# Kernel tuning notes

Measured on AMD Instinct MI355X. Metric: run time of the kernel, lower is better.

The kernel has to match this reference:

```python
import jax, jax.numpy as jnp
import numpy as np


def _dwconv(x, w, pad):
    # x: [B,C,H,W], w: [C,1,kh,kw] depthwise conv (groups=C), no bias
    return jax.lax.conv_general_dilated(
        x, w, window_strides=(1, 1), padding=[(pad, pad), (pad, pad)],
        dimension_numbers=('NCHW', 'OIHW', 'NCHW'),
        feature_group_count=x.shape[1])


def _omni_shift(x, alpha, cw1, cw3, cw5):
    # OmniShift training branch: alpha-weighted identity + 1x1 + 3x3 + 5x5 depthwise convs
    return (alpha[0] * x + alpha[1] * _dwconv(x, cw1, 0)
            + alpha[2] * _dwconv(x, cw3, 1) + alpha[3] * _dwconv(x, cw5, 2))


def _wkv(w_dec, u, k, v):
    # Numerically-stable RWKV-v4 WKV recurrence. w_dec,u: [D]; k,v: [B,T,D]
    kT = jnp.swapaxes(k, 0, 1)  # [T,B,D]
    vT = jnp.swapaxes(v, 0, 1)
    z = jnp.zeros_like(k[:, 0])
    init = (z, z, jnp.full_like(z, -1e38))  # (a, b, running max exponent)

    def step(carry, kv):
        a, b, pp = carry
        kt, vt = kv
        ww = u + kt
        p = jnp.maximum(pp, ww)
        e1 = jnp.exp(pp - p)
        e2 = jnp.exp(ww - p)
        out = (e1 * a + e2 * vt) / (e1 * b + e2)
        ww2 = pp + w_dec
        p2 = jnp.maximum(ww2, kt)
        f1 = jnp.exp(ww2 - p2)
        f2 = jnp.exp(kt - p2)
        return (f1 * a + f2 * vt, f1 * b + f2, p2), out

    _, out = jax.lax.scan(step, init, (kT, vT))
    return jnp.swapaxes(out, 0, 1)


def _forward(x, alpha, cw1, cw3, cw5, Wk, Wv, Wr, Wo, spatial_decay, spatial_first, h, w):
    B, T, C = x.shape
    xi = x.reshape(B, h, w, C).transpose(0, 3, 1, 2)  # b (h w) c -> b c h w
    xi = _omni_shift(xi, alpha, cw1, cw3, cw5)
    xf = xi.transpose(0, 2, 3, 1).reshape(B, T, C)    # b c h w -> b (h w) c
    k = jnp.einsum('btc,oc->bto', xf, Wk)
    v = jnp.einsum('btc,oc->bto', xf, Wv)
    r = jnp.einsum('btc,oc->bto', xf, Wr)
    sr = jax.nn.sigmoid(r)
    # 'b (h w) c -> b (w h) c' : W-major reordering for the second scan direction
    k1 = k.reshape(B, h, w, C).transpose(0, 2, 1, 3).reshape(B, T, C)
    v1 = v.reshape(B, h, w, C).transpose(0, 2, 1, 3).reshape(B, T, C)
    ks = jnp.concatenate([k, k1], axis=2)   # [B,T,2C]
    vs = jnp.concatenate([v, v1], axis=2)
    srs = jnp.concatenate([sr, sr], axis=2)
    w_dec = -jnp.exp(spatial_decay / T)  # WKV kernel applies w = -exp(w)
    u = spatial_first / T
    xs = _wkv(w_dec, u, ks, vs)
    xs = xs * srs
    return jnp.einsum('btd,cd->btc', xs, Wo)  # output Linear(2C -> C), no bias


def setup_inputs() -> dict:
    key = jax.random.key(0)
    ks = jax.random.split(key, 11)
    B, h, w, C = 8, 64, 64, 256
    T = h * w
    s = 0.02
    return {
        'x': jax.random.normal(ks[0], (B, T, C), jnp.float32),
        'alpha': jax.random.normal(ks[1], (4,), jnp.float32),
        'cw1': jax.random.normal(ks[2], (C, 1, 1, 1), jnp.float32) * s,
        'cw3': jax.random.normal(ks[3], (C, 1, 3, 3), jnp.float32) * s,
        'cw5': jax.random.normal(ks[4], (C, 1, 5, 5), jnp.float32) * s,
        'Wk': jax.random.normal(ks[5], (C, C), jnp.float32) * s,
        'Wv': jax.random.normal(ks[6], (C, C), jnp.float32) * s,
        'Wr': jax.random.normal(ks[7], (C, C), jnp.float32) * s,
        'Wo': jax.random.normal(ks[8], (C, 2 * C), jnp.float32) * s,
        'spatial_decay': jax.random.normal(ks[9], (2 * C,), jnp.float32),
        'spatial_first': jax.random.normal(ks[10], (2 * C,), jnp.float32),
        'h': h,
        'w': w,
    }


def reference(x, alpha, cw1, cw3, cw5, Wk, Wv, Wr, Wo, spatial_decay, spatial_first, h, w):
    return _forward(x, alpha, cw1, cw3, cw5, Wk, Wv, Wr, Wo, spatial_decay, spatial_first, h, w)
```

## Files before the change

### kernel.cpp

```cpp
#include <hip/hip_runtime.h>
#include <math.h>
#include <stdint.h>

#define TT 4096
#define HH 64
#define WW 64
#define CC 256
#define NCH 64
#define LCH 64

typedef __bf16 bf16x8 __attribute__((ext_vector_type(8)));
typedef float  f32x4  __attribute__((ext_vector_type(4)));

__device__ __forceinline__ unsigned short f2bf(float x) {
    uint32_t u = __float_as_uint(x);
    u = (u + 0x7fffu + ((u >> 16) & 1u)) >> 16;
    return (unsigned short)u;
}
__device__ __forceinline__ float bf2f(unsigned short h) {
    return __uint_as_float(((uint32_t)h) << 16);
}

__global__ __launch_bounds__(256)
void prep_all(const float* __restrict__ alpha,
              const float* __restrict__ cw1,
              const float* __restrict__ cw3,
              const float* __restrict__ cw5,
              const float* __restrict__ Wk, const float* __restrict__ Wv,
              const float* __restrict__ Wr, const float* __restrict__ Wo,
              float* __restrict__ weff,
              unsigned short* __restrict__ W2k, unsigned short* __restrict__ W2v,
              unsigned short* __restrict__ W2r, unsigned short* __restrict__ Wo2,
              int do_wo) {
    int bid = blockIdx.x, c = threadIdx.x;
    if (bid < 25) {
        int k = bid;
        float a0 = alpha[0], a1 = alpha[1], a2 = alpha[2], a3 = alpha[3];
        float v = a3 * cw5[c * 25 + k];
        int ky = k / 5, kx = k % 5;
        if (ky >= 1 && ky <= 3 && kx >= 1 && kx <= 3)
            v += a2 * cw3[c * 9 + (ky - 1) * 3 + (kx - 1)];
        if (k == 12) v += a1 * cw1[c] + a0;
        weff[k * CC + c] = v;
    } else if (bid < 281) {
        int n = bid - 25;
        float a;
        unsigned short h;
        a = Wk[n * 256 + c]; h = f2bf(a); W2k[n * 512 + c] = h; W2k[n * 512 + 256 + c] = f2bf(a - bf2f(h));
        a = Wv[n * 256 + c]; h = f2bf(a); W2v[n * 512 + c] = h; W2v[n * 512 + 256 + c] = f2bf(a - bf2f(h));
        a = Wr[n * 256 + c]; h = f2bf(a); W2r[n * 512 + c] = h; W2r[n * 512 + 256 + c] = f2bf(a - bf2f(h));
    } else if (do_wo) {
        int n = bid - 281;
        float a = Wo[n * 512 + c];
        unsigned short h = f2bf(a);
        Wo2[n * 1024 + c] = h; Wo2[n * 1024 + 256 + c] = f2bf(a - bf2f(h));
        float b = Wo[n * 512 + 256 + c];
        unsigned short h2 = f2bf(b);
        Wo2[n * 1024 + 512 + c] = h2; Wo2[n * 1024 + 768 + c] = f2bf(b - bf2f(h2));
    }
}

__global__ __launch_bounds__(256)
void prep_wo(const float* __restrict__ Wo, unsigned short* __restrict__ Wo2) {
    int n = blockIdx.x, c = threadIdx.x;
    float a = Wo[n * 512 + c];
    unsigned short h = f2bf(a);
    Wo2[n * 1024 + c] = h; Wo2[n * 1024 + 256 + c] = f2bf(a - bf2f(h));
    float b = Wo[n * 512 + 256 + c];
    unsigned short h2 = f2bf(b);
    Wo2[n * 1024 + 512 + c] = h2; Wo2[n * 1024 + 768 + c] = f2bf(b - bf2f(h2));
}

__global__ __launch_bounds__(256)
void omni_conv(const float* __restrict__ x,
               const float* __restrict__ weff,
               unsigned short* __restrict__ A2) {
    int xx = blockIdx.x;
    int y0 = blockIdx.y * 32;
    int b  = blockIdx.z;
    int c  = threadIdx.x;
    const float* xb = x + (size_t)b * TT * CC + c;
    unsigned short* Ab = A2 + (size_t)b * TT * 512 + c;

    float wk[25];
    #pragma unroll
    for (int k = 0; k < 25; ++k) wk[k] = weff[k * CC + c];

    float win[5][5];
    #pragma unroll
    for (int i = 0; i < 4; ++i) {
        int yy = y0 - 2 + i;
        #pragma unroll
        for (int dx = 0; dx < 5; ++dx) {
            int xc = xx + dx - 2;
            win[i][dx] = (yy >= 0 && xc >= 0 && xc < WW)
                         ? xb[(size_t)(yy * WW + xc) * CC] : 0.f;
        }
    }
    #pragma unroll
    for (int i = 0; i < 32; ++i) {
        int y = y0 + i;
        int yy = y + 2;
        #pragma unroll
        for (int dx = 0; dx < 5; ++dx) {
            int xc = xx + dx - 2;
            win[4][dx] = (yy < HH && xc >= 0 && xc < WW)
                         ? xb[(size_t)(yy * WW + xc) * CC] : 0.f;
        }
        float acc = 0.f;
        #pragma unroll
        for (int r = 0; r < 5; ++r)
            #pragma unroll
            for (int dx = 0; dx < 5; ++dx)
                acc = fmaf(wk[r * 5 + dx], win[r][dx], acc);
        unsigned short h = f2bf(acc);
        size_t o = (size_t)(y * WW + xx) * 512;
        Ab[o] = h;
        Ab[o + 256] = f2bf(acc - bf2f(h));
        #pragma unroll
        for (int r = 0; r < 4; ++r)
            #pragma unroll
            for (int dx = 0; dx < 5; ++dx)
                win[r][dx] = win[r + 1][dx];
    }
}

template<int KIND>
__device__ __forceinline__ void mfma_core(const unsigned short* __restrict__ A0,
                                          const unsigned short* __restrict__ A1,
                                          const unsigned short* __restrict__ W2,
                                          float* __restrict__ C,
                                          int m_blk, int n_blk, bool act) {
    __shared__ __align__(16) unsigned short L[2][4][128 * 32];
    int tid = threadIdx.x;
    int w = tid >> 6, l = tid & 63;
    int q = l >> 4, rr = l & 15;
    int wm = (w & 1) * 64, wn = (w >> 1) * 64;
    int srw = w * 16 + (l >> 2);
    int ss  = l & 3;

    const int NCHK = (KIND == 0) ? 8 : 16;
    const int LDW  = (KIND == 0) ? 512 : 1024;

    f32x4 acc[4][4];
    #pragma unroll
    for (int i = 0; i < 4; ++i)
        #pragma unroll
        for (int j = 0; j < 4; ++j)
            acc[i][j] = (f32x4){0.f, 0.f, 0.f, 0.f};

    auto stage = [&](int cc, int buf) {
        const unsigned short* Ab;
        int ah, al, wh, wl;
        if (KIND == 0) {
            Ab = A0; ah = cc * 32; al = 256 + cc * 32;
            wh = cc * 32; wl = 256 + cc * 32;
        } else {
            int c8 = cc & 7;
            Ab = (cc < 8) ? A0 : A1;
            ah = c8 * 32; al = 256 + c8 * 32;
            wh = ((cc < 8) ? 0 : 512) + c8 * 32;
            wl = ((cc < 8) ? 256 : 768) + c8 * 32;
        }
        #pragma unroll
        for (int i = 0; i < 2; ++i) {
            int r = i * 64 + srw;
            int sl = (ss ^ ((r >> 1) & 3)) * 8;
            size_t arow = (size_t)(m_blk + r) * 512;
            size_t wrow = (size_t)(n_blk + r) * LDW;
            int db = (i * 64 + w * 16) * 32;
            __builtin_amdgcn_global_load_lds(
                (const __attribute__((address_space(1))) void*)(Ab + arow + ah + sl),
                (__attribute__((address_space(3))) void*)&L[buf][0][db], 16, 0, 0);
            __builtin_amdgcn_global_load_lds(
                (const __attribute__((address_space(1))) void*)(Ab + arow + al + sl),
                (__attribute__((address_space(3))) void*)&L[buf][1][db], 16, 0, 0);
            __builtin_amdgcn_global_load_lds(
                (const __attribute__((address_space(1))) void*)(W2 + wrow + wh + sl),
                (__attribute__((address_space(3))) void*)&L[buf][2][db], 16, 0, 0);
            __builtin_amdgcn_global_load_lds(
                (const __attribute__((address_space(1))) void*)(W2 + wrow + wl + sl),
                (__attribute__((address_space(3))) void*)&L[buf][3][db], 16, 0, 0);
        }
    };

    stage(0, 0);
    stage(1, 1);

    for (int cc = 0; cc < NCHK; ++cc) {
        int buf = cc & 1;
        if (cc + 1 < NCHK) {
            asm volatile("s_waitcnt vmcnt(8)" ::: "memory");
        } else {
            asm volatile("s_waitcnt vmcnt(0)" ::: "memory");
        }
        __builtin_amdgcn_s_barrier();

        bf16x8 ah4[4], al4[4], wh4[4], wl4[4];
        #pragma unroll
        for (int f = 0; f < 4; ++f) {
            int Ra = wm + f * 16 + rr;
            int sa = (q ^ ((Ra >> 1) & 3)) * 8;
            ah4[f] = *(const bf16x8*)&L[buf][0][Ra * 32 + sa];
            al4[f] = *(const bf16x8*)&L[buf][1][Ra * 32 + sa];
            int Rw = wn + f * 16 + rr;
            int sw2 = (q ^ ((Rw >> 1) & 3)) * 8;
            wh4[f] = *(const bf16x8*)&L[buf][2][Rw * 32 + sw2];
            wl4[f] = *(const bf16x8*)&L[buf][3][Rw * 32 + sw2];
        }
        __builtin_amdgcn_s_setprio(1);
        #pragma unroll
        for (int fm = 0; fm < 4; ++fm)
            #pragma unroll
            for (int fn = 0; fn < 4; ++fn)
                acc[fm][fn] = __builtin_amdgcn_mfma_f32_16x16x32_bf16(
                    ah4[fm], wh4[fn], acc[fm][fn], 0, 0, 0);
        #pragma unroll
        for (int fm = 0; fm < 4; ++fm)
            #pragma unroll
            for (int fn = 0; fn < 4; ++fn)
                acc[fm][fn] = __builtin_amdgcn_mfma_f32_16x16x32_bf16(
                    al4[fm], wh4[fn], acc[fm][fn], 0, 0, 0);
        #pragma unroll
        for (int fm = 0; fm < 4; ++fm)
            #pragma unroll
            for (int fn = 0; fn < 4; ++fn)
                acc[fm][fn] = __builtin_amdgcn_mfma_f32_16x16x32_bf16(
                    ah4[fm], wl4[fn], acc[fm][fn], 0, 0, 0);
        __builtin_amdgcn_s_setprio(0);

        __builtin_amdgcn_s_barrier();
        if (cc + 2 < NCHK) stage(cc + 2, buf);
    }

    #pragma unroll
    for (int fm = 0; fm < 4; ++fm)
        #pragma unroll
        for (int fn = 0; fn < 4; ++fn) {
            int col = n_blk + wn + fn * 16 + rr;
            int row0 = m_blk + wm + fm * 16 + q * 4;
            f32x4 v = acc[fm][fn];
            #pragma unroll
            for (int j = 0; j < 4; ++j) {
                float o = v[j];
                if (act) o = 1.f / (1.f + __expf(-o));
                C[(size_t)(row0 + j) * 256 + col] = o;
            }
        }
}

__global__ __launch_bounds__(256, 2)
void gemm_kvr_mfma(const unsigned short* __restrict__ A2,
                   const unsigned short* __restrict__ W2k,
                   const unsigned short* __restrict__ W2v,
                   const unsigned short* __restrict__ W2r,
                   float* __restrict__ kb, float* __restrict__ vb,
                   float* __restrict__ rb) {
    int id = blockIdx.x;
    int xcd = id & 7;
    int j = id >> 3;
    int v = j % 6;
    int mq = j / 6;
    int m_blk = (mq * 8 + xcd) * 128;
    int mat = v >> 1;
    int n_blk = (v & 1) * 128;
    const unsigned short* W2 = (mat == 0) ? W2k : (mat == 1) ? W2v : W2r;
    float* C = (mat == 0) ? kb : (mat == 1) ? vb : rb;
    mfma_core<0>(A2, A2, W2, C, m_blk, n_blk, mat == 2);
}

__global__ __launch_bounds__(256, 2)
void gemm_out_mfma(const unsigned short* __restrict__ xs0,
                   const unsigned short* __restrict__ xs1,
                   const unsigned short* __restrict__ Wo2,
                   float* __restrict__ out) {
    int id = blockIdx.x;
    int xcd = id & 7;
    int j = id >> 3;
    int v = j & 1;
    int mq = j >> 1;
    int m_blk = (mq * 8 + xcd) * 128;
    mfma_core<1>(xs0, xs1, Wo2, out, m_blk, v * 128, false);
}

__global__ __launch_bounds__(256)
void wkv_pass1(const float* __restrict__ kin, const float* __restrict__ vin,
               const float* __restrict__ sdecay,
               float* __restrict__ cs_a, float* __restrict__ cs_b,
               float* __restrict__ cs_p) {
    int ch = blockIdx.x, dir = blockIdx.y, bb = blockIdx.z, c = threadIdx.x;
    float wd = -expf(sdecay[dir * CC + c] * (1.f / TT));
    const float* kb = kin + (size_t)bb * TT * CC + c;
    const float* vb = vin + (size_t)bb * TT * CC + c;
    float a = 0.f, b = 0.f, p = -1e38f;
    for (int i0 = 0; i0 < LCH; i0 += 8) {
        float k8[8], v8[8];
        #pragma unroll
        for (int i = 0; i < 8; ++i) {
            int ii = i0 + i;
            int src = dir ? (ii * WW + ch) : (ch * LCH + ii);
            k8[i] = kb[(size_t)src * CC];
            v8[i] = vb[(size_t)src * CC];
        }
        #pragma unroll
        for (int i = 0; i < 8; ++i) {
            float kt = k8[i], vt = v8[i];
            float ww2 = p + wd;
            float p2 = fmaxf(ww2, kt);
            float f1 = __expf(ww2 - p2), f2 = __expf(kt - p2);
            a = f1 * a + f2 * vt; b = f1 * b + f2; p = p2;
        }
    }
    size_t o = ((size_t)(bb * 2 + dir) * NCH + ch) * CC + c;
    cs_a[o] = a; cs_b[o] = b; cs_p[o] = p;
}

__global__ __launch_bounds__(256)
void wkv_pass3(const float* __restrict__ kin, const float* __restrict__ vin,
               const float* __restrict__ srin,
               const float* __restrict__ sdecay, const float* __restrict__ sfirst,
               const float* __restrict__ cs_a, const float* __restrict__ cs_b,
               const float* __restrict__ cs_p,
               unsigned short* __restrict__ xs2_0, unsigned short* __restrict__ xs2_1) {
    int ch = blockIdx.x, dir = blockIdx.y, bb = blockIdx.z, c = threadIdx.x;
    int d = dir * CC + c;
    float u  = sfirst[d] * (1.f / TT);
    float wd = -expf(sdecay[d] * (1.f / TT));
    float Ld = (float)LCH * wd;

    float a = 0.f, b = 0.f, p = -1e38f;
    size_t base = (size_t)(bb * 2 + dir) * NCH * CC + c;
    for (int j = 0; j < ch; ++j) {
        size_t o = base + (size_t)j * CC;
        float al = cs_a[o], bl = cs_b[o], pl = cs_p[o];
        float sh = p + Ld;
        float pn = fmaxf(sh, pl);
        float e1 = __expf(sh - pn), e2 = __expf(pl - pn);
        a = e1 * a + e2 * al; b = e1 * b + e2 * bl; p = pn;
    }

    const float* kb  = kin  + (size_t)bb * TT * CC + c;
    const float* vb  = vin  + (size_t)bb * TT * CC + c;
    const float* srb = srin + (size_t)bb * TT * CC + c;
    unsigned short* xo = (dir ? xs2_1 : xs2_0) + (size_t)bb * TT * 512 + c;
    for (int i0 = 0; i0 < LCH; i0 += 8) {
        float k8[8], v8[8], s8[8];
        #pragma unroll
        for (int i = 0; i < 8; ++i) {
            int ii = i0 + i;
            int t = ch * LCH + ii;
            int src = dir ? (ii * WW + ch) : t;
            k8[i] = kb[(size_t)src * CC];
            v8[i] = vb[(size_t)src * CC];
            s8[i] = srb[(size_t)t * CC];
        }
        #pragma unroll
        for (int i = 0; i < 8; ++i) {
            int t = ch * LCH + i0 + i;
            float kt = k8[i], vt = v8[i];
            float ww = u + kt;
            float qq = fmaxf(p, ww);
            float e1 = __expf(p - qq), e2 = __expf(ww - qq);
            float out = (e1 * a + e2 * vt) / (e1 * b + e2);
            float os = out * s8[i];
            unsigned short h = f2bf(os);
            xo[(size_t)t * 512] = h;
            xo[(size_t)t * 512 + 256] = f2bf(os - bf2f(h));
            float ww2 = p + wd;
            float p2  = fmaxf(ww2, kt);
            float f1 = __expf(ww2 - p2), f2 = __expf(kt - p2);
            a = f1 * a + f2 * vt; b = f1 * b + f2; p = p2;
        }
    }
}

extern "C" void kernel_launch(void* const* d_in, const int* in_sizes, int n_in,
                              void* d_out, int out_size, void* d_ws, size_t ws_size,
                              hipStream_t stream) {
    const float* x     = (const float*)d_in[0];
    const float* alpha = (const float*)d_in[1];
    const float* cw1   = (const float*)d_in[2];
    const float* cw3   = (const float*)d_in[3];
    const float* cw5   = (const float*)d_in[4];
    const float* Wk    = (const float*)d_in[5];
    const float* Wv    = (const float*)d_in[6];
    const float* Wr    = (const float*)d_in[7];
    const float* Wo    = (const float*)d_in[8];
    const float* sd    = (const float*)d_in[9];
    const float* sf    = (const float*)d_in[10];
    (void)n_in; (void)out_size;

    int B = in_sizes[0] / (TT * CC);
    int M = B * TT;
    size_t S = (size_t)M * 1024;

    char* wsb = (char*)d_ws;
    unsigned short* A2    = (unsigned short*)wsb;
    float*          kbuf  = (float*)(wsb + 1 * S);
    float*          vbuf  = (float*)(wsb + 2 * S);
    float*          srbuf = (float*)(wsb + 3 * S);
    unsigned short* xs2_1 = (unsigned short*)(wsb + 4 * S);
    unsigned short* xs2_0 = A2;

    bool wo_early = (ws_size >= 5 * S + 524288);
    unsigned short* Wo2 = wo_early ? (unsigned short*)(wsb + 5 * S)
                                   : (unsigned short*)(wsb + 3 * S);

    size_t SC = (size_t)B * 2 * NCH * CC;
    char* ob = (char*)d_out;
    float* cs_a = (float*)ob;
    float* cs_b = (float*)(ob + SC * 4);
    float* cs_p = (float*)(ob + 2 * SC * 4);
    float* weff = (float*)(ob + 3 * SC * 4);
    unsigned short* W2k = (unsigned short*)(ob + (4u << 20));
    unsigned short* W2v = (unsigned short*)(ob + (4u << 20) + 262144);
    unsigned short* W2r = (unsigned short*)(ob + (4u << 20) + 524288);

    prep_all<<<537, CC, 0, stream>>>(alpha, cw1, cw3, cw5, Wk, Wv, Wr, Wo,
                                     weff, W2k, W2v, W2r, Wo2,
                                     wo_early ? 1 : 0);
    omni_conv<<<dim3(WW, 2, B), CC, 0, stream>>>(x, weff, A2);

    gemm_kvr_mfma<<<(M / 128) * 6, 256, 0, stream>>>(A2, W2k, W2v, W2r,
                                                     kbuf, vbuf, srbuf);

    wkv_pass1<<<dim3(NCH, 2, B), 256, 0, stream>>>(kbuf, vbuf, sd, cs_a, cs_b, cs_p);
    wkv_pass3<<<dim3(NCH, 2, B), 256, 0, stream>>>(kbuf, vbuf, srbuf, sd, sf,
                                                   cs_a, cs_b, cs_p, xs2_0, xs2_1);

    if (!wo_early)
        prep_wo<<<256, CC, 0, stream>>>(Wo, Wo2);
    gemm_out_mfma<<<(M / 128) * 2, 256, 0, stream>>>(xs2_0, xs2_1, Wo2,
                                                     (float*)d_out);
}
```

Measured before the change: 276.7 us.

## Add parallel chunk-state scan kernel and interleave two chunks per WKV thread

Moves the serial cross-chunk prefix combine out of wkv_pass3 into a new wkv_scan2 kernel that does a 64-lane log-step shuffle scan over chunk states and writes exclusive prefixes. This removes the quadratic serial loop in which late chunks re-walked every earlier chunk. pass1 and pass3 now each handle two independent chunks per thread, giving two interleaved recurrences for ILP at half the grid size. The division is replaced by a raw v_rcp_f32, which trades a little precision for fewer instructions. The change adds one kernel launch and halves the block count.

New measurement: 283.0 us. 1.02x slower.

```diff
diff --git a/kernel.cpp b/kernel.cpp
--- a/kernel.cpp
+++ b/kernel.cpp
@@ -19,6 +19,11 @@
 }
 __device__ __forceinline__ float bf2f(unsigned short h) {
     return __uint_as_float(((uint32_t)h) << 16);
+}
+__device__ __forceinline__ float fast_rcp(float x) {
+    float r;
+    asm("v_rcp_f32 %0, %1" : "=v"(r) : "v"(x));
+    return r;
 }
 
 __global__ __launch_bounds__(256)
@@ -288,31 +293,75 @@
                const float* __restrict__ sdecay,
                float* __restrict__ cs_a, float* __restrict__ cs_b,
                float* __restrict__ cs_p) {
-    int ch = blockIdx.x, dir = blockIdx.y, bb = blockIdx.z, c = threadIdx.x;
+    int chA = blockIdx.x, dir = blockIdx.y, bb = blockIdx.z, c = threadIdx.x;
+    int chB = chA + NCH / 2;
     float wd = -expf(sdecay[dir * CC + c] * (1.f / TT));
     const float* kb = kin + (size_t)bb * TT * CC + c;
     const float* vb = vin + (size_t)bb * TT * CC + c;
-    float a = 0.f, b = 0.f, p = -1e38f;
+    float aA = 0.f, bA = 0.f, pA = -1e38f;
+    float aB = 0.f, bB = 0.f, pB = -1e38f;
     for (int i0 = 0; i0 < LCH; i0 += 8) {
-        float k8[8], v8[8];
+        float kA8[8], vA8[8], kB8[8], vB8[8];
         #pragma unroll
         for (int i = 0; i < 8; ++i) {
             int ii = i0 + i;
-            int src = dir ? (ii * WW + ch) : (ch * LCH + ii);
-            k8[i] = kb[(size_t)src * CC];
-            v8[i] = vb[(size_t)src * CC];
+            int sA = dir ? (ii * WW + chA) : (chA * LCH + ii);
+            int sB = dir ? (ii * WW + chB) : (chB * LCH + ii);
+            kA8[i] = kb[(size_t)sA * CC]; vA8[i] = vb[(size_t)sA * CC];
+            kB8[i] = kb[(size_t)sB * CC]; vB8[i] = vb[(size_t)sB * CC];
         }
         #pragma unroll
         for (int i = 0; i < 8; ++i) {
-            float kt = k8[i], vt = v8[i];
-            float ww2 = p + wd;
-            float p2 = fmaxf(ww2, kt);
-            float f1 = __expf(ww2 - p2), f2 = __expf(kt - p2);
-            a = f1 * a + f2 * vt; b = f1 * b + f2; p = p2;
-        }
-    }
-    size_t o = ((size_t)(bb * 2 + dir) * NCH + ch) * CC + c;
-    cs_a[o] = a; cs_b[o] = b; cs_p[o] = p;
+            {
+                float kt = kA8[i], vt = vA8[i];
+                float ww2 = pA + wd;
+                float p2 = fmaxf(ww2, kt);
+                float f1 = __expf(ww2 - p2), f2 = __expf(kt - p2);
+                aA = f1 * aA + f2 * vt; bA = f1 * bA + f2; pA = p2;
+            }
+            {
+                float kt = kB8[i], vt = vB8[i];
+                float ww2 = pB + wd;
+                float p2 = fmaxf(ww2, kt);
+                float f1 = __expf(ww2 - p2), f2 = __expf(kt - p2);
+                aB = f1 * aB + f2 * vt; bB = f1 * bB + f2; pB = p2;
+            }
+        }
+    }
+    size_t base = (size_t)(bb * 2 + dir) * NCH * CC + c;
+    size_t oA = base + (size_t)chA * CC, oB = base + (size_t)chB * CC;
+    cs_a[oA] = aA; cs_b[oA] = bA; cs_p[oA] = pA;
+    cs_a[oB] = aB; cs_b[oB] = bB; cs_p[oB] = pB;
+}
+
+__global__ __launch_bounds__(64)
+void wkv_scan2(const float* __restrict__ sdecay,
+               float* __restrict__ cs_a, float* __restrict__ cs_b,
+               float* __restrict__ cs_p) {
+    int c = blockIdx.x, dir = blockIdx.y, bb = blockIdx.z;
+    int lane = threadIdx.x;
+    float wd = -expf(sdecay[dir * CC + c] * (1.f / TT));
+    float Ld = (float)LCH * wd;
+    size_t o = (size_t)(bb * 2 + dir) * NCH * CC + (size_t)lane * CC + c;
+    float a = cs_a[o], b = cs_b[o], p = cs_p[o];
+    #pragma unroll
+    for (int s = 0; s < 6; ++s) {
+        int dlt = 1 << s;
+        float xa = __shfl_up(a, dlt, 64);
+        float xb = __shfl_up(b, dlt, 64);
+        float xp = __shfl_up(p, dlt, 64);
+        if (lane >= dlt) {
+            float sh = xp + Ld * (float)dlt;
+            float pn = fmaxf(sh, p);
+            float e1 = __expf(sh - pn), e2 = __expf(p - pn);
+            a = e1 * xa + e2 * a; b = e1 * xb + e2 * b; p = pn;
+        }
+    }
+    float ea = __shfl_up(a, 1, 64);
+    float eb = __shfl_up(b, 1, 64);
+    float ep = __shfl_up(p, 1, 64);
+    if (lane == 0) { ea = 0.f; eb = 0.f; ep = -1e38f; }
+    cs_a[o] = ea; cs_b[o] = eb; cs_p[o] = ep;
 }
 
 __global__ __launch_bounds__(256)
@@ -322,54 +371,69 @@
                const float* __restrict__ cs_a, const float* __restrict__ cs_b,
                const float* __restrict__ cs_p,
                unsigned short* __restrict__ xs2_0, unsigned short* __restrict__ xs2_1) {
-    int ch = blockIdx.x, dir = blockIdx.y, bb = blockIdx.z, c = threadIdx.x;
+    int chA = blockIdx.x, dir = blockIdx.y, bb = blockIdx.z, c = threadIdx.x;
+    int chB = chA + NCH / 2;
     int d = dir * CC + c;
     float u  = sfirst[d] * (1.f / TT);
     float wd = -expf(sdecay[d] * (1.f / TT));
-    float Ld = (float)LCH * wd;
-
-    float a = 0.f, b = 0.f, p = -1e38f;
     size_t base = (size_t)(bb * 2 + dir) * NCH * CC + c;
-    for (int j = 0; j < ch; ++j) {
-        size_t o = base + (size_t)j * CC;
-        float al = cs_a[o], bl = cs_b[o], pl = cs_p[o];
-        float sh = p + Ld;
-        float pn = fmaxf(sh, pl);
-        float e1 = __expf(sh - pn), e2 = __expf(pl - pn);
-        a = e1 * a + e2 * al; b = e1 * b + e2 * bl; p = pn;
-    }
-
+    size_t oA = base + (size_t)chA * CC, oB = base + (size_t)chB * CC;
+    float aA = cs_a[oA], bA = cs_b[oA], pA = cs_p[oA];
+    float aB = cs_a[oB], bB = cs_b[oB], pB = cs_p[oB];
     const float* kb  = kin  + (size_t)bb * TT * CC + c;
     const float* vb  = vin  + (size_t)bb * TT * CC + c;
     const float* srb = srin + (size_t)bb * TT * CC + c;
     unsigned short* xo = (dir ? xs2_1 : xs2_0) + (size_t)bb * TT * 512 + c;
     for (int i0 = 0; i0 < LCH; i0 += 8) {
-        float k8[8], v8[8], s8[8];
+        float kA8[8], vA8[8], sA8[8], kB8[8], vB8[8], sB8[8];
         #pragma unroll
         for (int i = 0; i < 8; ++i) {
             int ii = i0 + i;
-            int t = ch * LCH + ii;
-            int src = dir ? (ii * WW + ch) : t;
-            k8[i] = kb[(size_t)src * CC];
-            v8[i] = vb[(size_t)src * CC];
-            s8[i] = srb[(size_t)t * CC];
+            int tA = chA * LCH + ii;
+            int tB = chB * LCH + ii;
+            int sA = dir ? (ii * WW + chA) : tA;
+            int sB = dir ? (ii * WW + chB) : tB;
+            kA8[i] = kb[(size_t)sA * CC]; vA8[i] = vb[(size_t)sA * CC];
+            sA8[i] = srb[(size_t)tA * CC];
+            kB8[i] = kb[(size_t)sB * CC]; vB8[i] = vb[(size_t)sB * CC];
+            sB8[i] = srb[(size_t)tB * CC];
         }
         #pragma unroll
         for (int i = 0; i < 8; ++i) {
-            int t = ch * LCH + i0 + i;
-            float kt = k8[i], vt = v8[i];
-            float ww = u + kt;
-            float qq = fmaxf(p, ww);
-            float e1 = __expf(p - qq), e2 = __expf(ww - qq);
-            float out = (e1 * a + e2 * vt) / (e1 * b + e2);
-            float os = out * s8[i];
-            unsigned short h = f2bf(os);
-            xo[(size_t)t * 512] = h;
-            xo[(size_t)t * 512 + 256] = f2bf(os - bf2f(h));
-            float ww2 = p + wd;
-            float p2  = fmaxf(ww2, kt);
-            float f1 = __expf(ww2 - p2), f2 = __expf(kt - p2);
-            a = f1 * a + f2 * vt; b = f1 * b + f2; p = p2;
+            {
+                int t = chA * LCH + i0 + i;
+                float kt = kA8[i], vt = vA8[i];
+                float ww = u + kt;
+                float qq = fmaxf(pA, ww);
+                float e1 = __expf(pA - qq), e2 = __expf(ww - qq);
+                float num = e1 * aA + e2 * vt;
+                float den = e1 * bA + e2;
+                float os = num * fast_rcp(den) * sA8[i];
+                unsigned short h = f2bf(os);
+                xo[(size_t)t * 512] = h;
+                xo[(size_t)t * 512 + 256] = f2bf(os - bf2f(h));
+                float ww2 = pA + wd;
+                float p2  = fmaxf(ww2, kt);
+                float f1 = __expf(ww2 - p2), f2 = __expf(kt - p2);
+                aA = f1 * aA + f2 * vt; bA = f1 * bA + f2; pA = p2;
+            }
+            {
+                int t = chB * LCH + i0 + i;
+                float kt = kB8[i], vt = vB8[i];
+                float ww = u + kt;
+                float qq = fmaxf(pB, ww);
+                float e1 = __expf(pB - qq), e2 = __expf(ww - qq);
+                float num = e1 * aB + e2 * vt;
+                float den = e1 * bB + e2;
+                float os = num * fast_rcp(den) * sB8[i];
+                unsigned short h = f2bf(os);
+                xo[(size_t)t * 512] = h;
+                xo[(size_t)t * 512 + 256] = f2bf(os - bf2f(h));
+                float ww2 = pB + wd;
+                float p2  = fmaxf(ww2, kt);
+                float f1 = __expf(ww2 - p2), f2 = __expf(kt - p2);
+                aB = f1 * aB + f2 * vt; bB = f1 * bB + f2; pB = p2;
+            }
         }
     }
 }
@@ -424,9 +488,12 @@
     gemm_kvr_mfma<<<(M / 128) * 6, 256, 0, stream>>>(A2, W2k, W2v, W2r,
                                                      kbuf, vbuf, srbuf);
 
-    wkv_pass1<<<dim3(NCH, 2, B), 256, 0, stream>>>(kbuf, vbuf, sd, cs_a, cs_b, cs_p);
-    wkv_pass3<<<dim3(NCH, 2, B), 256, 0, stream>>>(kbuf, vbuf, srbuf, sd, sf,
-                                                   cs_a, cs_b, cs_p, xs2_0, xs2_1);
+    wkv_pass1<<<dim3(NCH / 2, 2, B), 256, 0, stream>>>(kbuf, vbuf, sd,
+                                                       cs_a, cs_b, cs_p);
+    wkv_scan2<<<dim3(CC, 2, B), 64, 0, stream>>>(sd, cs_a, cs_b, cs_p);
+    wkv_pass3<<<dim3(NCH / 2, 2, B), 256, 0, stream>>>(kbuf, vbuf, srbuf, sd, sf,
+                                                       cs_a, cs_b, cs_p,
+                                                       xs2_0, xs2_1);
 
     if (!wo_early)
         prep_wo<<<256, CC, 0, stream>>>(Wo, Wo2);
```
